# Kernel tuning notes

Measured on AMD Instinct MI355X. Metric: run time of the kernel, lower is better.

## Reference

```python
import jax, jax.numpy as jnp
import numpy as np

H = W = 20
NVARS = 4          # n_predictor_vars
NK = 12            # n_conv2d_kernels
NF = NK + NVARS + 1  # 17 augmented channels (conv + original + time)
SIGLEN = NF + NF * NF  # 306, depth-2 signature length
T_END = 1.0        # self.T in the module


def setup_inputs() -> dict:
    key = jax.random.key(0)
    ks = jax.random.split(key, 8)
    B, T = 64, 96
    x = jax.random.normal(ks[0], (B, T, NVARS, H, W), dtype=jnp.float32)
    conv_w = jax.random.normal(ks[1], (NK, NVARS, 3, 3), dtype=jnp.float32) * 0.1
    conv_b = jax.random.normal(ks[2], (NK,), dtype=jnp.float32) * 0.01
    d_in = SIGLEN * H * W  # 122400

    def lin(k, fan_in, fan_out):
        return jax.random.normal(k, (fan_in, fan_out), dtype=jnp.float32) / np.float32(np.sqrt(fan_in))

    w1, b1 = lin(ks[3], d_in, 32), jnp.zeros((32,), jnp.float32)
    w2, b2 = lin(ks[4], 32, 32), jnp.zeros((32,), jnp.float32)
    w3, b3 = lin(ks[5], 32, 32), jnp.zeros((32,), jnp.float32)
    w4, b4 = lin(ks[6], 32, 1), jnp.zeros((1,), jnp.float32)
    return {"x": x, "conv_w": conv_w, "conv_b": conv_b,
            "w1": w1, "b1": b1, "w2": w2, "b2": b2,
            "w3": w3, "b3": b3, "w4": w4, "b4": b4}


def reference(x, conv_w, conv_b, w1, b1, w2, b2, w3, b3, w4, b4):
    B, T = x.shape[0], x.shape[1]
    # Batched conv over all timesteps at once (the torch code loops over t).
    xi = x.reshape(B * T, NVARS, H, W)
    y = jax.lax.conv_general_dilated(
        xi, conv_w, window_strides=(1, 1), padding='SAME',
        dimension_numbers=('NCHW', 'OIHW', 'NCHW'))
    y = y + conv_b[None, :, None, None]
    y = y.reshape(B, T, NK, H, W)
    # Dropout3d is identity in eval mode.
    # Augment: [conv features, original values, time channel] along channel dim.
    tch = jnp.linspace(0.0, T_END, T, dtype=x.dtype).reshape(1, T, 1, 1, 1)
    tch = jnp.broadcast_to(tch, (B, T, 1, H, W))
    feat = jnp.concatenate([y, x, tch], axis=2)        # (B, T, NF, H, W)
    path = jnp.transpose(feat, (0, 3, 4, 1, 2))        # (B, H, W, T, NF)
    # Depth-2 path signature (Chen closed form):
    # level1 = sum dx; level2 = sum_{i<j} dx_i (x) dx_j + 0.5 sum_i dx_i (x) dx_i
    dx = path[..., 1:, :] - path[..., :-1, :]          # (B,H,W,T-1,NF)
    csum = jnp.cumsum(dx, axis=-2)                     # inclusive prefix sums
    lvl1 = csum[..., -1, :]                            # (B,H,W,NF)
    # (exclusive prefix) + 0.5*dx = csum - 0.5*dx -> single contracted einsum
    lvl2 = jnp.einsum('bhwti,bhwtj->bhwij', csum - 0.5 * dx, dx)
    sig = jnp.concatenate([lvl1, lvl2.reshape(B, H, W, NF * NF)], axis=-1)  # (B,H,W,306)
    flat = sig.reshape(B, H * W * SIGLEN)
    h = jax.nn.relu(flat @ w1 + b1)
    h = jax.nn.relu(h @ w2 + b2)
    h = jax.nn.relu(h @ w3 + b3)
    return h @ w4 + b4                                 # (B, 1)
```

## Files before the change

kernel.cpp:

```cpp
#include <hip/hip_runtime.h>

#define HH 20
#define WW 20
#define TT 96
#define BB 64
#define SIG 306
#define NFC 17
#define FROW 16
#define PIXSTRIDE 260
#define CHUNK 16
#define NCHUNK 6
#define XT 199
#define KTOT 122400
#define KSLAB 120
#define NSLAB 4
#define NKBLK 255

__global__ __launch_bounds__(64) void prep_weights(
    const float* __restrict__ cw, float* __restrict__ cwr)
{
  const int i = threadIdx.x;
  #pragma unroll
  for (int r = 0; r < 7; r++) {
    int idx = r * 64 + i;
    if (idx < 432) {
      int ci = idx / 108, r2 = idx % 108, dy = r2 / 36, r3 = r2 % 36;
      int k = r3 / 3, dx = r3 % 3;
      cwr[idx] = cw[k * 36 + ci * 9 + dy * 3 + dx];
    }
  }
}

__global__ __launch_bounds__(256) void sig_kernel(
    const float* __restrict__ x,
    const float* __restrict__ cwr,
    float* __restrict__ sig)
{
  __shared__ __align__(16) float feat[16 * PIXSTRIDE];
  __shared__ __align__(16) float xs[CHUNK * XT];

  const int tid = threadIdx.x;
  const int blk = blockIdx.x;
  const int b = blk / 25;
  const int tile = blk % 25;
  const int th4 = (tile / 5) * 4, tw4 = (tile % 5) * 4;
  const float* xb0 = x + (size_t)b * TT * 1600;

  int g_off[9], l_off[9];
  #pragma unroll
  for (int r = 0; r < 9; r++) {
    int idx = r * 256 + tid;
    int t = idx / 144, q = idx % 144;
    int ci = q / 36, pos = q % 36, row = pos / 6, col = pos % 6;
    int gr = th4 - 1 + row, gc = tw4 - 1 + col;
    bool valid = (gr >= 0 && gr < HH && gc >= 0 && gc < WW);
    g_off[r] = valid ? (t * 1600 + ci * 400 + gr * WW + gc) : -1;
    l_off[r] = t * XT + ci * 48 + row * 8 + col;
  }

  const int cpix = tid >> 4, ctt = tid & 15;
  const int cpy = cpix >> 2, cpx = cpix & 3;

  const int p2 = tid >> 4;
  const int rr = tid & 15, it = rr >> 2, jt = rr & 3;
  const int i0 = it * 4, j0 = jt * 4;

  float accv[4][4];
  float f0a[4], f0b[4], pa[4], pb[4], fsum[4];
  #pragma unroll
  for (int i = 0; i < 4; i++) {
    f0a[i] = 0.f; f0b[i] = 0.f; pa[i] = 0.f; pb[i] = 0.f; fsum[i] = 0.f;
    #pragma unroll
    for (int j = 0; j < 4; j++) accv[i][j] = 0.f;
  }

  for (int chunk = 0; chunk < NCHUNK; chunk++) {
    {
      const float* xbc = xb0 + (size_t)chunk * CHUNK * 1600;
      float rg[9];
      #pragma unroll
      for (int r = 0; r < 9; r++)
        rg[r] = (g_off[r] >= 0) ? xbc[g_off[r]] : 0.f;
      #pragma unroll
      for (int r = 0; r < 9; r++) xs[l_off[r]] = rg[r];
    }
    __syncthreads();

    {
      float win[4][9];
      const int wb2 = ctt * XT;
      #pragma unroll
      for (int ci = 0; ci < 4; ci++)
        #pragma unroll
        for (int dy = 0; dy < 3; dy++)
          #pragma unroll
          for (int dxx = 0; dxx < 3; dxx++)
            win[ci][dy * 3 + dxx] = xs[wb2 + ci * 48 + (cpy + dy) * 8 + (cpx + dxx)];

      float fk[12];
      #pragma unroll
      for (int k = 0; k < 12; k++) fk[k] = 0.f;
      #pragma unroll
      for (int ci = 0; ci < 4; ci++) {
        #pragma unroll
        for (int dy = 0; dy < 3; dy++) {
          const float* wp = cwr + (ci * 3 + dy) * 36;
          const float w0a = win[ci][dy * 3 + 0];
          const float w1a = win[ci][dy * 3 + 1];
          const float w2a = win[ci][dy * 3 + 2];
          #pragma unroll
          for (int k = 0; k < 12; k++)
            fk[k] += w0a * wp[k * 3 + 0] + w1a * wp[k * 3 + 1] + w2a * wp[k * 3 + 2];
        }
      }
      float* fr = &feat[cpix * PIXSTRIDE + ctt * FROW];
      *reinterpret_cast<float4*>(fr + 0)  = make_float4(fk[0], fk[1], fk[2], fk[3]);
      *reinterpret_cast<float4*>(fr + 4)  = make_float4(fk[4], fk[5], fk[6], fk[7]);
      *reinterpret_cast<float4*>(fr + 8)  = make_float4(fk[8], fk[9], fk[10], fk[11]);
      *reinterpret_cast<float4*>(fr + 12) = make_float4(win[0][4], win[1][4], win[2][4], win[3][4]);
    }
    __syncthreads();

    int tstart = 0;
    if (chunk == 0) {
      const float* r0 = &feat[p2 * PIXSTRIDE];
      const float4 a4 = *reinterpret_cast<const float4*>(r0 + i0);
      const float4 b4 = *reinterpret_cast<const float4*>(r0 + j0);
      f0a[0] = a4.x; f0a[1] = a4.y; f0a[2] = a4.z; f0a[3] = a4.w;
      f0b[0] = b4.x; f0b[1] = b4.y; f0b[2] = b4.z; f0b[3] = b4.w;
      #pragma unroll
      for (int i = 0; i < 4; i++) { pa[i] = f0a[i]; pb[i] = f0b[i]; fsum[i] = f0a[i]; }
      tstart = 1;
    }

    for (int tt = tstart; tt < CHUNK; tt++) {
      const float* row = &feat[p2 * PIXSTRIDE + tt * FROW];
      const float4 a4 = *reinterpret_cast<const float4*>(row + i0);
      const float4 b4 = *reinterpret_cast<const float4*>(row + j0);
      float fa[4] = {a4.x, a4.y, a4.z, a4.w};
      float fb[4] = {b4.x, b4.y, b4.z, b4.w};
      float av[4], bv[4];
      #pragma unroll
      for (int i = 0; i < 4; i++) {
        av[i] = 0.5f * (fa[i] + pa[i]) - f0a[i];
        bv[i] = fb[i] - pb[i];
        fsum[i] += fa[i];
        pa[i] = fa[i]; pb[i] = fb[i];
      }
      #pragma unroll
      for (int i = 0; i < 4; i++)
        #pragma unroll
        for (int j = 0; j < 4; j++) accv[i][j] += av[i] * bv[j];
    }
    __syncthreads();
  }

  {
    const int ph = th4 + (p2 >> 2), pw = tw4 + (p2 & 3);
    float* sb = sig + (size_t)b * KTOT + (size_t)(ph * WW + pw) * SIG;
    #pragma unroll
    for (int ii = 0; ii < 4; ii++)
      #pragma unroll
      for (int jj = 0; jj < 4; jj++)
        sb[NFC + (i0 + ii) * NFC + (j0 + jj)] = accv[ii][jj];
    if (jt == 0) {
      #pragma unroll
      for (int ii = 0; ii < 4; ii++) {
        const int c = i0 + ii;
        const float f0 = f0a[ii], f95 = pa[ii], fs = fsum[ii];
        sb[c] = f95 - f0;
        sb[NFC + c * NFC + 16] = (fs - 95.5f * f0 - 0.5f * f95) * (1.f / 95.f);
        sb[NFC + 16 * NFC + c] = (95.5f * f95 + 0.5f * f0 - fs) * (1.f / 95.f);
      }
      if (it == 0) { sb[16] = 1.0f; sb[NFC + 16 * NFC + 16] = 0.5f; }
    }
  }
}

template<bool ATOMIC>
__global__ __launch_bounds__(256) void mlp1_gemm(
    const float* __restrict__ sig, const float* __restrict__ w1,
    float* __restrict__ part)
{
  __shared__ __align__(16) float ldsT[KSLAB * 68];
  __shared__ __align__(16) float wls[KSLAB * 32];
  const int tid = threadIdx.x;
  const int n = tid & 31, bq = tid >> 5;
  const int k0 = blockIdx.x * (KSLAB * NSLAB);

  float a8[8];
  #pragma unroll
  for (int i = 0; i < 8; i++) a8[i] = 0.f;

  for (int s = 0; s < NSLAB; s++) {
    const int ks = k0 + s * KSLAB;
    __syncthreads();
    #pragma unroll
    for (int r = 0; r < 30; r++) {
      int idx = r * 256 + tid;
      int b = idx / KSLAB, kk = idx % KSLAB;
      ldsT[kk * 68 + b] = sig[(size_t)b * KTOT + ks + kk];
    }
    #pragma unroll
    for (int r = 0; r < 15; r++) {
      int idx = r * 256 + tid;
      wls[idx] = w1[(size_t)ks * 32 + idx];
    }
    __syncthreads();

    #pragma unroll 4
    for (int kk = 0; kk < KSLAB; kk++) {
      const float w = wls[kk * 32 + n];
      const float4 s0 = *reinterpret_cast<const float4*>(&ldsT[kk * 68 + bq * 8]);
      const float4 s1 = *reinterpret_cast<const float4*>(&ldsT[kk * 68 + bq * 8 + 4]);
      a8[0] += s0.x * w; a8[1] += s0.y * w; a8[2] += s0.z * w; a8[3] += s0.w * w;
      a8[4] += s1.x * w; a8[5] += s1.y * w; a8[6] += s1.z * w; a8[7] += s1.w * w;
    }
  }

  if (ATOMIC) {
    #pragma unroll
    for (int i = 0; i < 8; i++)
      atomicAdd(&part[(bq * 8 + i) * 32 + n], a8[i]);
  } else {
    const size_t pb = (size_t)blockIdx.x * (BB * 32);
    #pragma unroll
    for (int i = 0; i < 8; i++)
      part[pb + (bq * 8 + i) * 32 + n] = a8[i];
  }
}

__global__ __launch_bounds__(256) void mlp_tail(
    const float* __restrict__ part, int npart, const float* __restrict__ b1,
    const float* __restrict__ w2, const float* __restrict__ b2,
    const float* __restrict__ w3, const float* __restrict__ b3,
    const float* __restrict__ w4, const float* __restrict__ b4,
    float* __restrict__ out)
{
  const int tid = threadIdx.x;
  const int n = tid & 31;
  const int b = blockIdx.x * 8 + (tid >> 5);
  const int lane = tid & 63;
  const int grp = lane & 32;

  float s = 0.f;
  #pragma unroll 4
  for (int p = 0; p < npart; p++)
    s += part[(size_t)p * (BB * 32) + b * 32 + n];

  float h = fmaxf(s + b1[n], 0.f);

  float v = b2[n];
  #pragma unroll
  for (int k = 0; k < 32; k++)
    v += __shfl(h, grp + k, 64) * w2[k * 32 + n];
  h = fmaxf(v, 0.f);

  v = b3[n];
  #pragma unroll
  for (int k = 0; k < 32; k++)
    v += __shfl(h, grp + k, 64) * w3[k * 32 + n];
  h = fmaxf(v, 0.f);

  float p = h * w4[n];
  #pragma unroll
  for (int o = 16; o >= 1; o >>= 1) p += __shfl_xor(p, o, 64);
  if (n == 0) out[b] = p + b4[0];
}

extern "C" void kernel_launch(void* const* d_in, const int* in_sizes, int n_in,
                              void* d_out, int out_size, void* d_ws, size_t ws_size,
                              hipStream_t stream) {
  const float* x  = (const float*)d_in[0];
  const float* cw = (const float*)d_in[1];
  const float* b1 = (const float*)d_in[4];
  const float* w1 = (const float*)d_in[3];
  const float* w2 = (const float*)d_in[5];
  const float* b2 = (const float*)d_in[6];
  const float* w3 = (const float*)d_in[7];
  const float* b3 = (const float*)d_in[8];
  const float* w4 = (const float*)d_in[9];
  const float* b4 = (const float*)d_in[10];
  float* out = (float*)d_out;

  const size_t sig_bytes  = (size_t)BB * KTOT * sizeof(float);
  const size_t part_bytes = (size_t)NKBLK * BB * 32 * sizeof(float);
  float* sigm = (float*)d_ws;

  if (ws_size >= sig_bytes + part_bytes + 2048) {
    float* part = (float*)((char*)d_ws + sig_bytes);
    float* cwr  = (float*)((char*)d_ws + sig_bytes + part_bytes);
    prep_weights<<<dim3(1), dim3(64), 0, stream>>>(cw, cwr);
    sig_kernel<<<dim3(1600), dim3(256), 0, stream>>>(x, cwr, sigm);
    mlp1_gemm<false><<<dim3(NKBLK), dim3(256), 0, stream>>>(sigm, w1, part);
    mlp_tail<<<dim3(8), dim3(256), 0, stream>>>(part, NKBLK, b1, w2, b2, w3, b3, w4, b4, out);
  } else {
    float* acc = (float*)((char*)d_ws + sig_bytes);
    float* cwr = (float*)((char*)d_ws + sig_bytes + 8192);
    prep_weights<<<dim3(1), dim3(64), 0, stream>>>(cw, cwr);
    hipMemsetAsync(acc, 0, BB * 32 * sizeof(float), stream);
    sig_kernel<<<dim3(1600), dim3(256), 0, stream>>>(x, cwr, sigm);
    mlp1_gemm<true><<<dim3(NKBLK), dim3(256), 0, stream>>>(sigm, w1, acc);
    mlp_tail<<<dim3(8), dim3(256), 0, stream>>>(acc, 1, b1, w2, b2, w3, b3, w4, b4, out);
  }
}
```

Baseline: 275.8 us.

## Fuse conv weight prep into sig kernel, restructure feature layout and split GEMM finer

Removes the separate prep_weights launch by loading the conv weights into shared memory inside the signature kernel, padded to float4 rows. The feature buffer becomes time-major with a padded stride, and the level-2 recurrence is reformulated algebraically (sum of adjacent features times the difference, with the f0 correction applied at the end), using vector stores for the output. The time loops are fully unrolled and chunk 0 is peeled, and the first MLP GEMM uses half the K slab so twice as many blocks run. These changes aim to cut launch overhead, LDS bank conflicts and per-step arithmetic, at the cost of more partial sums to reduce in the tail.

```diff
diff --git a/kernel.cpp b/kernel.cpp
--- a/kernel.cpp
+++ b/kernel.cpp
@@ -6,38 +6,25 @@
 #define BB 64
 #define SIG 306
 #define NFC 17
-#define FROW 16
-#define PIXSTRIDE 260
+#define TSTRIDE 264
 #define CHUNK 16
 #define NCHUNK 6
 #define XT 199
 #define KTOT 122400
 #define KSLAB 120
-#define NSLAB 4
-#define NKBLK 255
-
-__global__ __launch_bounds__(64) void prep_weights(
-    const float* __restrict__ cw, float* __restrict__ cwr)
-{
-  const int i = threadIdx.x;
-  #pragma unroll
-  for (int r = 0; r < 7; r++) {
-    int idx = r * 64 + i;
-    if (idx < 432) {
-      int ci = idx / 108, r2 = idx % 108, dy = r2 / 36, r3 = r2 % 36;
-      int k = r3 / 3, dx = r3 % 3;
-      cwr[idx] = cw[k * 36 + ci * 9 + dy * 3 + dx];
-    }
-  }
-}
+#define NSLAB 2
+#define NKBLK 510
+
+typedef float float4u __attribute__((ext_vector_type(4), aligned(4)));
 
 __global__ __launch_bounds__(256) void sig_kernel(
     const float* __restrict__ x,
-    const float* __restrict__ cwr,
+    const float* __restrict__ cw,
     float* __restrict__ sig)
 {
-  __shared__ __align__(16) float feat[16 * PIXSTRIDE];
+  __shared__ __align__(16) float feat[15 * TSTRIDE + 256 + 8];
   __shared__ __align__(16) float xs[CHUNK * XT];
+  __shared__ __align__(16) float wlds[12 * 48];
 
   const int tid = threadIdx.x;
   const int blk = blockIdx.x;
@@ -45,6 +32,16 @@
   const int tile = blk % 25;
   const int th4 = (tile / 5) * 4, tw4 = (tile % 5) * 4;
   const float* xb0 = x + (size_t)b * TT * 1600;
+
+  #pragma unroll
+  for (int r = 0; r < 3; r++) {
+    int idx = r * 256 + tid;
+    if (idx < 576) {
+      int k = idx / 48, rem = idx % 48;
+      int ci = rem / 12, r2 = rem % 12, dy = r2 >> 2, dx = r2 & 3;
+      wlds[idx] = (dx < 3) ? cw[k * 36 + ci * 9 + dy * 3 + dx] : 0.f;
+    }
+  }
 
   int g_off[9], l_off[9];
   #pragma unroll
@@ -69,100 +66,111 @@
   float f0a[4], f0b[4], pa[4], pb[4], fsum[4];
   #pragma unroll
   for (int i = 0; i < 4; i++) {
-    f0a[i] = 0.f; f0b[i] = 0.f; pa[i] = 0.f; pb[i] = 0.f; fsum[i] = 0.f;
     #pragma unroll
     for (int j = 0; j < 4; j++) accv[i][j] = 0.f;
   }
 
-  for (int chunk = 0; chunk < NCHUNK; chunk++) {
-    {
-      const float* xbc = xb0 + (size_t)chunk * CHUNK * 1600;
-      float rg[9];
-      #pragma unroll
-      for (int r = 0; r < 9; r++)
-        rg[r] = (g_off[r] >= 0) ? xbc[g_off[r]] : 0.f;
-      #pragma unroll
-      for (int r = 0; r < 9; r++) xs[l_off[r]] = rg[r];
-    }
-    __syncthreads();
-
-    {
-      float win[4][9];
-      const int wb2 = ctt * XT;
-      #pragma unroll
-      for (int ci = 0; ci < 4; ci++)
+  auto stage = [&](int chunk) {
+    const float* xbc = xb0 + (size_t)chunk * CHUNK * 1600;
+    float rg[9];
+    #pragma unroll
+    for (int r = 0; r < 9; r++)
+      rg[r] = (g_off[r] >= 0) ? xbc[g_off[r]] : 0.f;
+    #pragma unroll
+    for (int r = 0; r < 9; r++) xs[l_off[r]] = rg[r];
+  };
+
+  auto conv = [&]() {
+    float win[4][9];
+    const int wb2 = ctt * XT;
+    #pragma unroll
+    for (int ci = 0; ci < 4; ci++)
+      #pragma unroll
+      for (int dy = 0; dy < 3; dy++)
         #pragma unroll
-        for (int dy = 0; dy < 3; dy++)
-          #pragma unroll
-          for (int dxx = 0; dxx < 3; dxx++)
-            win[ci][dy * 3 + dxx] = xs[wb2 + ci * 48 + (cpy + dy) * 8 + (cpx + dxx)];
-
-      float fk[12];
-      #pragma unroll
-      for (int k = 0; k < 12; k++) fk[k] = 0.f;
+        for (int dxx = 0; dxx < 3; dxx++)
+          win[ci][dy * 3 + dxx] = xs[wb2 + ci * 48 + (cpy + dy) * 8 + (cpx + dxx)];
+
+    float fk[12];
+    #pragma unroll
+    for (int k = 0; k < 12; k++) {
+      float a = 0.f;
       #pragma unroll
       for (int ci = 0; ci < 4; ci++) {
         #pragma unroll
         for (int dy = 0; dy < 3; dy++) {
-          const float* wp = cwr + (ci * 3 + dy) * 36;
-          const float w0a = win[ci][dy * 3 + 0];
-          const float w1a = win[ci][dy * 3 + 1];
-          const float w2a = win[ci][dy * 3 + 2];
-          #pragma unroll
-          for (int k = 0; k < 12; k++)
-            fk[k] += w0a * wp[k * 3 + 0] + w1a * wp[k * 3 + 1] + w2a * wp[k * 3 + 2];
+          const float4 w4 = *reinterpret_cast<const float4*>(
+              &wlds[k * 48 + ci * 12 + dy * 4]);
+          a += win[ci][dy * 3 + 0] * w4.x + win[ci][dy * 3 + 1] * w4.y +
+               win[ci][dy * 3 + 2] * w4.z;
         }
       }
-      float* fr = &feat[cpix * PIXSTRIDE + ctt * FROW];
-      *reinterpret_cast<float4*>(fr + 0)  = make_float4(fk[0], fk[1], fk[2], fk[3]);
-      *reinterpret_cast<float4*>(fr + 4)  = make_float4(fk[4], fk[5], fk[6], fk[7]);
-      *reinterpret_cast<float4*>(fr + 8)  = make_float4(fk[8], fk[9], fk[10], fk[11]);
-      *reinterpret_cast<float4*>(fr + 12) = make_float4(win[0][4], win[1][4], win[2][4], win[3][4]);
-    }
-    __syncthreads();
-
-    int tstart = 0;
-    if (chunk == 0) {
-      const float* r0 = &feat[p2 * PIXSTRIDE];
-      const float4 a4 = *reinterpret_cast<const float4*>(r0 + i0);
-      const float4 b4 = *reinterpret_cast<const float4*>(r0 + j0);
-      f0a[0] = a4.x; f0a[1] = a4.y; f0a[2] = a4.z; f0a[3] = a4.w;
-      f0b[0] = b4.x; f0b[1] = b4.y; f0b[2] = b4.z; f0b[3] = b4.w;
-      #pragma unroll
-      for (int i = 0; i < 4; i++) { pa[i] = f0a[i]; pb[i] = f0b[i]; fsum[i] = f0a[i]; }
-      tstart = 1;
-    }
-
-    for (int tt = tstart; tt < CHUNK; tt++) {
-      const float* row = &feat[p2 * PIXSTRIDE + tt * FROW];
-      const float4 a4 = *reinterpret_cast<const float4*>(row + i0);
-      const float4 b4 = *reinterpret_cast<const float4*>(row + j0);
-      float fa[4] = {a4.x, a4.y, a4.z, a4.w};
-      float fb[4] = {b4.x, b4.y, b4.z, b4.w};
-      float av[4], bv[4];
-      #pragma unroll
-      for (int i = 0; i < 4; i++) {
-        av[i] = 0.5f * (fa[i] + pa[i]) - f0a[i];
-        bv[i] = fb[i] - pb[i];
-        fsum[i] += fa[i];
-        pa[i] = fa[i]; pb[i] = fb[i];
-      }
-      #pragma unroll
-      for (int i = 0; i < 4; i++)
-        #pragma unroll
-        for (int j = 0; j < 4; j++) accv[i][j] += av[i] * bv[j];
-    }
-    __syncthreads();
+      fk[k] = a;
+    }
+    float* fr = &feat[ctt * TSTRIDE + cpix * 16];
+    *reinterpret_cast<float4*>(fr + 0)  = make_float4(fk[0], fk[1], fk[2], fk[3]);
+    *reinterpret_cast<float4*>(fr + 4)  = make_float4(fk[4], fk[5], fk[6], fk[7]);
+    *reinterpret_cast<float4*>(fr + 8)  = make_float4(fk[8], fk[9], fk[10], fk[11]);
+    *reinterpret_cast<float4*>(fr + 12) = make_float4(win[0][4], win[1][4], win[2][4], win[3][4]);
+  };
+
+  auto p2step = [&](int tt) {
+    const float* row = &feat[tt * TSTRIDE + p2 * 16];
+    const float4 a4 = *reinterpret_cast<const float4*>(row + i0);
+    const float4 b4 = *reinterpret_cast<const float4*>(row + j0);
+    float fa[4] = {a4.x, a4.y, a4.z, a4.w};
+    float fb[4] = {b4.x, b4.y, b4.z, b4.w};
+    float sa[4], db[4];
+    #pragma unroll
+    for (int i = 0; i < 4; i++) { sa[i] = fa[i] + pa[i]; db[i] = fb[i] - pb[i]; }
+    #pragma unroll
+    for (int i = 0; i < 4; i++)
+      #pragma unroll
+      for (int j = 0; j < 4; j++) accv[i][j] += sa[i] * db[j];
+    #pragma unroll
+    for (int i = 0; i < 4; i++) { fsum[i] += fa[i]; pa[i] = fa[i]; pb[i] = fb[i]; }
+  };
+
+  stage(0);
+  __syncthreads();
+  conv();
+  __syncthreads();
+  {
+    const float* r0 = &feat[p2 * 16];
+    const float4 a4 = *reinterpret_cast<const float4*>(r0 + i0);
+    const float4 b4 = *reinterpret_cast<const float4*>(r0 + j0);
+    f0a[0] = a4.x; f0a[1] = a4.y; f0a[2] = a4.z; f0a[3] = a4.w;
+    f0b[0] = b4.x; f0b[1] = b4.y; f0b[2] = b4.z; f0b[3] = b4.w;
+    #pragma unroll
+    for (int i = 0; i < 4; i++) { pa[i] = f0a[i]; pb[i] = f0b[i]; fsum[i] = f0a[i]; }
+  }
+  #pragma unroll
+  for (int tt = 1; tt < CHUNK; tt++) p2step(tt);
+
+  for (int chunk = 1; chunk < NCHUNK; chunk++) {
+    __syncthreads();
+    stage(chunk);
+    __syncthreads();
+    conv();
+    __syncthreads();
+    #pragma unroll
+    for (int tt = 0; tt < CHUNK; tt++) p2step(tt);
   }
 
   {
     const int ph = th4 + (p2 >> 2), pw = tw4 + (p2 & 3);
     float* sb = sig + (size_t)b * KTOT + (size_t)(ph * WW + pw) * SIG;
-    #pragma unroll
-    for (int ii = 0; ii < 4; ii++)
+    float lv1b[4];
+    #pragma unroll
+    for (int j = 0; j < 4; j++) lv1b[j] = pb[j] - f0b[j];
+    #pragma unroll
+    for (int ii = 0; ii < 4; ii++) {
+      float4u v;
       #pragma unroll
       for (int jj = 0; jj < 4; jj++)
-        sb[NFC + (i0 + ii) * NFC + (j0 + jj)] = accv[ii][jj];
+        v[jj] = 0.5f * accv[ii][jj] - f0a[ii] * lv1b[jj];
+      *reinterpret_cast<float4u*>(sb + NFC + (i0 + ii) * NFC + j0) = v;
+    }
     if (jt == 0) {
       #pragma unroll
       for (int ii = 0; ii < 4; ii++) {
@@ -273,8 +281,8 @@
                               hipStream_t stream) {
   const float* x  = (const float*)d_in[0];
   const float* cw = (const float*)d_in[1];
+  const float* w1 = (const float*)d_in[3];
   const float* b1 = (const float*)d_in[4];
-  const float* w1 = (const float*)d_in[3];
   const float* w2 = (const float*)d_in[5];
   const float* b2 = (const float*)d_in[6];
   const float* w3 = (const float*)d_in[7];
@@ -287,19 +295,15 @@
   const size_t part_bytes = (size_t)NKBLK * BB * 32 * sizeof(float);
   float* sigm = (float*)d_ws;
 
-  if (ws_size >= sig_bytes + part_bytes + 2048) {
+  sig_kernel<<<dim3(1600), dim3(256), 0, stream>>>(x, cw, sigm);
+
+  if (ws_size >= sig_bytes + part_bytes) {
     float* part = (float*)((char*)d_ws + sig_bytes);
-    float* cwr  = (float*)((char*)d_ws + sig_bytes + part_bytes);
-    prep_weights<<<dim3(1), dim3(64), 0, stream>>>(cw, cwr);
-    sig_kernel<<<dim3(1600), dim3(256), 0, stream>>>(x, cwr, sigm);
     mlp1_gemm<false><<<dim3(NKBLK), dim3(256), 0, stream>>>(sigm, w1, part);
     mlp_tail<<<dim3(8), dim3(256), 0, stream>>>(part, NKBLK, b1, w2, b2, w3, b3, w4, b4, out);
   } else {
     float* acc = (float*)((char*)d_ws + sig_bytes);
-    float* cwr = (float*)((char*)d_ws + sig_bytes + 8192);
-    prep_weights<<<dim3(1), dim3(64), 0, stream>>>(cw, cwr);
     hipMemsetAsync(acc, 0, BB * 32 * sizeof(float), stream);
-    sig_kernel<<<dim3(1600), dim3(256), 0, stream>>>(x, cwr, sigm);
     mlp1_gemm<true><<<dim3(NKBLK), dim3(256), 0, stream>>>(sigm, w1, acc);
     mlp_tail<<<dim3(8), dim3(256), 0, stream>>>(acc, 1, b1, w2, b2, w3, b3, w4, b4, out);
   }
```

After: 283.4 us. 2.8% more time.
